# Performance work log

Hardware: AMD Instinct MI355X
Metric: run time of the kernel (lower is better)

Reference implementation:

```python
import jax, jax.numpy as jnp
import numpy as np

H_GRID = 512
W_GRID = 512
N_NODES = H_GRID * W_GRID


def gcn_conv(x, W, b, src, dst, n):
    # PyG GCNConv: linear transform, add self-loops, symmetric normalization,
    # scatter-add aggregation, bias.
    h = x @ W  # [N, F_out]
    # degree including self-loop (edge weights are all 1)
    deg = jax.ops.segment_sum(jnp.ones(src.shape[0], x.dtype), dst, num_segments=n) + 1.0
    dinv = jax.lax.rsqrt(deg)  # deg^-0.5
    norm = dinv[src] * dinv[dst]  # [E]
    msg = h[src] * norm[:, None]  # [E, F_out] gathered messages
    agg = jax.ops.segment_sum(msg, dst, num_segments=n)
    # self-loop contribution: norm_ii = deg_i^-0.5 * deg_i^-0.5 = 1/deg_i
    agg = agg + h * (dinv * dinv)[:, None]
    return agg + b


def setup_inputs() -> dict:
    key = jax.random.key(0)
    k_x, k_w1, k_w2, k_wfc = jax.random.split(key, 4)

    # 4-neighbor grid edges (both directions), matching build_grid_edges
    ii, jj = np.meshgrid(np.arange(H_GRID), np.arange(W_GRID), indexing='ij')
    idx = (ii * W_GRID + jj).astype(np.int32)
    src_h, dst_h = idx[:, :-1].ravel(), idx[:, 1:].ravel()
    src_v, dst_v = idx[:-1, :].ravel(), idx[1:, :].ravel()
    src = np.concatenate([src_h, dst_h, src_v, dst_v])
    dst = np.concatenate([dst_h, src_h, dst_v, src_v])
    edge_index = jnp.asarray(np.stack([src, dst]), dtype=jnp.int32)  # [2, E]

    x = jax.random.normal(k_x, (N_NODES, 2), dtype=jnp.float32)
    s1 = 1.0 / np.sqrt(2.0)
    s2 = 1.0 / np.sqrt(64.0)
    W1 = jax.random.uniform(k_w1, (2, 64), jnp.float32, -s1, s1)
    b1 = jnp.zeros((64,), jnp.float32)
    W2 = jax.random.uniform(k_w2, (64, 64), jnp.float32, -s2, s2)
    b2 = jnp.zeros((64,), jnp.float32)
    Wfc = jax.random.uniform(k_wfc, (64, 1), jnp.float32, -s2, s2)
    bfc = jnp.zeros((1,), jnp.float32)
    return {"x": x, "edge_index": edge_index, "W1": W1, "b1": b1,
            "W2": W2, "b2": b2, "Wfc": Wfc, "bfc": bfc}


def reference(x, edge_index, W1, b1, W2, b2, Wfc, bfc):
    src, dst = edge_index[0], edge_index[1]
    n = x.shape[0]
    h = jax.nn.relu(gcn_conv(x, W1, b1, src, dst, n))
    h = jax.nn.relu(gcn_conv(h, W2, b2, src, dst, n))
    out = jax.nn.sigmoid(h @ Wfc + bfc)  # [N, 1]
    return out.squeeze(-1)  # [N]
```

## Files before the change

kernel.cpp:

```cpp
#include <hip/hip_runtime.h>
#include <hip/hip_fp16.h>
#include <math.h>

#define HG 512
#define WG 512
#define F 64
#define TS 16
#define HS 18
#define HN (HS * HS)

typedef _Float16 f16x8 __attribute__((ext_vector_type(8)));
typedef __fp16 fp16x2 __attribute__((ext_vector_type(2)));
typedef __attribute__((ext_vector_type(4))) float f32x4;

__device__ __forceinline__ float dinv_of(int r, int c) {
    int nb = (r > 0) + (r < HG - 1) + (c > 0) + (c < WG - 1);
    return nb == 4 ? 0.4472135954999579f : (nb == 3 ? 0.5f : 0.5773502691896258f);
}

__device__ __forceinline__ int swz(int row, int ch) {
    int key = (row ^ (row >> 3)) & 7;
    return row * 128 + ((ch ^ key) << 4);
}

__device__ __forceinline__ __half2 bch2(unsigned u) { return __builtin_bit_cast(__half2, u); }

__global__ __launch_bounds__(1024, 8) void fused(const float* __restrict__ x,
                                                 const float* __restrict__ W1,
                                                 const float* __restrict__ b1,
                                                 const float* __restrict__ W2,
                                                 const float* __restrict__ b2,
                                                 const float* __restrict__ Wfc,
                                                 const float* __restrict__ bfc,
                                                 float* __restrict__ out) {
    __shared__ unsigned short Hs[HN * 64];
    __shared__ unsigned short WT[64 * 64];
    __shared__ float2 a1s[HN];

    char* hb = (char*)Hs;
    char* wb = (char*)WT;
    int tid = threadIdx.x;
    int tr = blockIdx.x >> 5, tc = blockIdx.x & 31;
    int r0 = tr * TS, c0 = tc * TS;

    for (int i = tid; i < 64 * 64; i += 1024) {
        int k = i >> 6, n = i & 63;
        *(_Float16*)(wb + swz(n, k >> 3) + (k & 7) * 2) = (_Float16)W2[i];
    }

    const float2* xv = (const float2*)x;
    if (tid < HN) {
        int node = tid;
        int lr = (node * 57) >> 10;
        int lc = node - lr * 18;
        int rT = r0 - 1 + lr, cT = c0 - 1 + lc;
        float s0 = 0.f, s1 = 0.f;
        if (rT >= 0 && rT < HG && cT >= 0 && cT < WG) {
            int n = (rT << 9) + cT;
            float di = dinv_of(rT, cT);
            float2 v = xv[n];
            s0 = di * di * v.x; s1 = di * di * v.y;
            if (cT > 0)      { float w = di * dinv_of(rT, cT - 1); float2 t = xv[n - 1];  s0 += w * t.x; s1 += w * t.y; }
            if (cT < WG - 1) { float w = di * dinv_of(rT, cT + 1); float2 t = xv[n + 1];  s0 += w * t.x; s1 += w * t.y; }
            if (rT > 0)      { float w = di * dinv_of(rT - 1, cT); float2 t = xv[n - WG]; s0 += w * t.x; s1 += w * t.y; }
            if (rT < HG - 1) { float w = di * dinv_of(rT + 1, cT); float2 t = xv[n + WG]; s0 += w * t.x; s1 += w * t.y; }
        }
        a1s[node] = make_float2(s0, s1);
    }

    int fq = tid & 15;
    float4 w0 = ((const float4*)W1)[fq];
    float4 w1 = ((const float4*)(W1 + 64))[fq];
    float4 bb = ((const float4*)b1)[fq];
    __syncthreads();
    for (int node = (tid >> 4); node < HN; node += 64) {
        float2 a = a1s[node];
        float h0 = fmaxf(fmaf(a.x, w0.x, fmaf(a.y, w1.x, bb.x)), 0.f);
        float h1v = fmaxf(fmaf(a.x, w0.y, fmaf(a.y, w1.y, bb.y)), 0.f);
        float h2 = fmaxf(fmaf(a.x, w0.z, fmaf(a.y, w1.z, bb.z)), 0.f);
        float h3 = fmaxf(fmaf(a.x, w0.w, fmaf(a.y, w1.w, bb.w)), 0.f);
        fp16x2 p0 = __builtin_amdgcn_cvt_pkrtz(h0, h1v);
        fp16x2 p1 = __builtin_amdgcn_cvt_pkrtz(h2, h3);
        uint2 pk;
        pk.x = __builtin_bit_cast(unsigned, p0);
        pk.y = __builtin_bit_cast(unsigned, p1);
        *(uint2*)(hb + swz(node, fq >> 1) + (fq & 1) * 8) = pk;
    }
    __syncthreads();

    int wv = tid >> 6, lane = tid & 63;
    int q = lane >> 4, col = lane & 15;

    int lr = wv + 1, lc = col + 1;
    int rT = r0 + wv, cT = c0 + col;
    float di = dinv_of(rT, cT);
    __half2 wc2 = __half2half2(__float2half(di * di));
    __half2 wl2 = __half2half2(__float2half((cT > 0)      ? di * dinv_of(rT, cT - 1) : 0.f));
    __half2 wr2 = __half2half2(__float2half((cT < WG - 1) ? di * dinv_of(rT, cT + 1) : 0.f));
    __half2 wu2 = __half2half2(__float2half((rT > 0)      ? di * dinv_of(rT - 1, cT) : 0.f));
    __half2 wd2 = __half2half2(__float2half((rT < HG - 1) ? di * dinv_of(rT + 1, cT) : 0.f));
    int hrow = lr * HS + lc;

    f16x8 af[2];
    #pragma unroll
    for (int ck = 0; ck < 2; ck++) {
        int c = ck * 4 + q;
        uint4 vc = *(const uint4*)(hb + swz(hrow, c));
        uint4 vl = *(const uint4*)(hb + swz(hrow - 1, c));
        uint4 vr = *(const uint4*)(hb + swz(hrow + 1, c));
        uint4 vu = *(const uint4*)(hb + swz(hrow - HS, c));
        uint4 vd = *(const uint4*)(hb + swz(hrow + HS, c));
        const unsigned* pc = (const unsigned*)&vc;
        const unsigned* pl = (const unsigned*)&vl;
        const unsigned* pr = (const unsigned*)&vr;
        const unsigned* pu = (const unsigned*)&vu;
        const unsigned* pd = (const unsigned*)&vd;
        unsigned res[4];
        #pragma unroll
        for (int u = 0; u < 4; u++) {
            __half2 a = __hmul2(bch2(pc[u]), wc2);
            a = __hfma2(bch2(pl[u]), wl2, a);
            a = __hfma2(bch2(pr[u]), wr2, a);
            a = __hfma2(bch2(pu[u]), wu2, a);
            a = __hfma2(bch2(pd[u]), wd2, a);
            res[u] = __builtin_bit_cast(unsigned, a);
        }
        uint4 r4 = {res[0], res[1], res[2], res[3]};
        af[ck] = __builtin_bit_cast(f16x8, r4);
    }

    float p[4] = {0.f, 0.f, 0.f, 0.f};
    #pragma unroll
    for (int nt = 0; nt < 4; nt++) {
        f16x8 bf0 = *(const f16x8*)(wb + swz(nt * 16 + col, q));
        f16x8 bf1 = *(const f16x8*)(wb + swz(nt * 16 + col, 4 + q));
        f32x4 z = {0.f, 0.f, 0.f, 0.f};
        z = __builtin_amdgcn_mfma_f32_16x16x32_f16(af[0], bf0, z, 0, 0, 0);
        z = __builtin_amdgcn_mfma_f32_16x16x32_f16(af[1], bf1, z, 0, 0, 0);
        float b2v = b2[nt * 16 + col];
        float wfv = Wfc[nt * 16 + col];
        #pragma unroll
        for (int rg = 0; rg < 4; rg++)
            p[rg] += fmaxf(z[rg] + b2v, 0.f) * wfv;
    }
    #pragma unroll
    for (int rg = 0; rg < 4; rg++) {
        #pragma unroll
        for (int s = 1; s < 16; s <<= 1)
            p[rg] += __shfl_xor(p[rg], s, 64);
    }
    if (col == 0) {
        float bfc0 = bfc[0];
        #pragma unroll
        for (int rg = 0; rg < 4; rg++) {
            int nT = (r0 + wv) * WG + c0 + q * 4 + rg;
            float zz = p[rg] + bfc0;
            out[nT] = 1.f / (1.f + expf(-zz));
        }
    }
}

extern "C" void kernel_launch(void* const* d_in, const int* in_sizes, int n_in,
                              void* d_out, int out_size, void* d_ws, size_t ws_size,
                              hipStream_t stream) {
    const float* x   = (const float*)d_in[0];
    const float* W1  = (const float*)d_in[2];
    const float* b1  = (const float*)d_in[3];
    const float* W2  = (const float*)d_in[4];
    const float* b2  = (const float*)d_in[5];
    const float* Wfc = (const float*)d_in[6];
    const float* bfc = (const float*)d_in[7];
    float* out = (float*)d_out;

    fused<<<(HG / TS) * (WG / TS), 1024, 0, stream>>>(x, W1, b1, W2, b2, Wfc, bfc, out);
}
```

Baseline: 86.66 us.

## Fuse layer-1 aggregation and transform, dropping the intermediate LDS buffer and barrier

Each thread now computes the 2-channel layer-1 aggregate for a node and directly applies W1, bias and ReLU for 8 output features, writing fp16 to the swizzled H tile. This removes the a1s shared buffer and one __syncthreads. Each node's aggregate is recomputed by 8 threads, adding redundant global loads and arithmetic. The W2 load is also vectorised as one float4 per thread and issued early to overlap with the stencil work.

```diff
diff --git a/kernel.cpp b/kernel.cpp
--- a/kernel.cpp
+++ b/kernel.cpp
@@ -24,6 +24,10 @@
 }
 
 __device__ __forceinline__ __half2 bch2(unsigned u) { return __builtin_bit_cast(__half2, u); }
+__device__ __forceinline__ unsigned pkrtz(float a, float b) {
+    fp16x2 p = __builtin_amdgcn_cvt_pkrtz(a, b);
+    return __builtin_bit_cast(unsigned, p);
+}
 
 __global__ __launch_bounds__(1024, 8) void fused(const float* __restrict__ x,
                                                  const float* __restrict__ W1,
@@ -35,7 +39,6 @@
                                                  float* __restrict__ out) {
     __shared__ unsigned short Hs[HN * 64];
     __shared__ unsigned short WT[64 * 64];
-    __shared__ float2 a1s[HN];
 
     char* hb = (char*)Hs;
     char* wb = (char*)WT;
@@ -43,55 +46,65 @@
     int tr = blockIdx.x >> 5, tc = blockIdx.x & 31;
     int r0 = tr * TS, c0 = tc * TS;
 
-    for (int i = tid; i < 64 * 64; i += 1024) {
-        int k = i >> 6, n = i & 63;
-        *(_Float16*)(wb + swz(n, k >> 3) + (k & 7) * 2) = (_Float16)W2[i];
+    float4 w2v = ((const float4*)W2)[tid];
+
+    int fh = tid & 7;
+    float4 wA0 = ((const float4*)W1)[2 * fh];
+    float4 wA1 = ((const float4*)W1)[2 * fh + 1];
+    float4 wB0 = ((const float4*)(W1 + 64))[2 * fh];
+    float4 wB1 = ((const float4*)(W1 + 64))[2 * fh + 1];
+    float4 bb0 = ((const float4*)b1)[2 * fh];
+    float4 bb1 = ((const float4*)b1)[2 * fh + 1];
+
+    const float2* xv = (const float2*)x;
+    #pragma unroll
+    for (int j = 0; j < 3; j++) {
+        int item = tid + j * 1024;
+        if (item < HN * 8) {
+            int node = item >> 3;
+            int lr = (node * 57) >> 10;
+            int lc = node - lr * 18;
+            int rT = r0 - 1 + lr, cT = c0 - 1 + lc;
+            float s0 = 0.f, s1 = 0.f;
+            if (rT >= 0 && rT < HG && cT >= 0 && cT < WG) {
+                int n = (rT << 9) + cT;
+                float di = dinv_of(rT, cT);
+                float2 v = xv[n];
+                s0 = di * di * v.x; s1 = di * di * v.y;
+                if (cT > 0)      { float w = di * dinv_of(rT, cT - 1); float2 t = xv[n - 1];  s0 += w * t.x; s1 += w * t.y; }
+                if (cT < WG - 1) { float w = di * dinv_of(rT, cT + 1); float2 t = xv[n + 1];  s0 += w * t.x; s1 += w * t.y; }
+                if (rT > 0)      { float w = di * dinv_of(rT - 1, cT); float2 t = xv[n - WG]; s0 += w * t.x; s1 += w * t.y; }
+                if (rT < HG - 1) { float w = di * dinv_of(rT + 1, cT); float2 t = xv[n + WG]; s0 += w * t.x; s1 += w * t.y; }
+            }
+            float h0 = fmaxf(fmaf(s0, wA0.x, fmaf(s1, wB0.x, bb0.x)), 0.f);
+            float h1v = fmaxf(fmaf(s0, wA0.y, fmaf(s1, wB0.y, bb0.y)), 0.f);
+            float h2 = fmaxf(fmaf(s0, wA0.z, fmaf(s1, wB0.z, bb0.z)), 0.f);
+            float h3 = fmaxf(fmaf(s0, wA0.w, fmaf(s1, wB0.w, bb0.w)), 0.f);
+            float h4 = fmaxf(fmaf(s0, wA1.x, fmaf(s1, wB1.x, bb1.x)), 0.f);
+            float h5 = fmaxf(fmaf(s0, wA1.y, fmaf(s1, wB1.y, bb1.y)), 0.f);
+            float h6 = fmaxf(fmaf(s0, wA1.z, fmaf(s1, wB1.z, bb1.z)), 0.f);
+            float h7 = fmaxf(fmaf(s0, wA1.w, fmaf(s1, wB1.w, bb1.w)), 0.f);
+            uint4 pk4;
+            pk4.x = pkrtz(h0, h1v);
+            pk4.y = pkrtz(h2, h3);
+            pk4.z = pkrtz(h4, h5);
+            pk4.w = pkrtz(h6, h7);
+            *(uint4*)(hb + swz(node, fh)) = pk4;
+        }
     }
 
-    const float2* xv = (const float2*)x;
-    if (tid < HN) {
-        int node = tid;
-        int lr = (node * 57) >> 10;
-        int lc = node - lr * 18;
-        int rT = r0 - 1 + lr, cT = c0 - 1 + lc;
-        float s0 = 0.f, s1 = 0.f;
-        if (rT >= 0 && rT < HG && cT >= 0 && cT < WG) {
-            int n = (rT << 9) + cT;
-            float di = dinv_of(rT, cT);
-            float2 v = xv[n];
-            s0 = di * di * v.x; s1 = di * di * v.y;
-            if (cT > 0)      { float w = di * dinv_of(rT, cT - 1); float2 t = xv[n - 1];  s0 += w * t.x; s1 += w * t.y; }
-            if (cT < WG - 1) { float w = di * dinv_of(rT, cT + 1); float2 t = xv[n + 1];  s0 += w * t.x; s1 += w * t.y; }
-            if (rT > 0)      { float w = di * dinv_of(rT - 1, cT); float2 t = xv[n - WG]; s0 += w * t.x; s1 += w * t.y; }
-            if (rT < HG - 1) { float w = di * dinv_of(rT + 1, cT); float2 t = xv[n + WG]; s0 += w * t.x; s1 += w * t.y; }
-        }
-        a1s[node] = make_float2(s0, s1);
-    }
-
-    int fq = tid & 15;
-    float4 w0 = ((const float4*)W1)[fq];
-    float4 w1 = ((const float4*)(W1 + 64))[fq];
-    float4 bb = ((const float4*)b1)[fq];
-    __syncthreads();
-    for (int node = (tid >> 4); node < HN; node += 64) {
-        float2 a = a1s[node];
-        float h0 = fmaxf(fmaf(a.x, w0.x, fmaf(a.y, w1.x, bb.x)), 0.f);
-        float h1v = fmaxf(fmaf(a.x, w0.y, fmaf(a.y, w1.y, bb.y)), 0.f);
-        float h2 = fmaxf(fmaf(a.x, w0.z, fmaf(a.y, w1.z, bb.z)), 0.f);
-        float h3 = fmaxf(fmaf(a.x, w0.w, fmaf(a.y, w1.w, bb.w)), 0.f);
-        fp16x2 p0 = __builtin_amdgcn_cvt_pkrtz(h0, h1v);
-        fp16x2 p1 = __builtin_amdgcn_cvt_pkrtz(h2, h3);
-        uint2 pk;
-        pk.x = __builtin_bit_cast(unsigned, p0);
-        pk.y = __builtin_bit_cast(unsigned, p1);
-        *(uint2*)(hb + swz(node, fq >> 1) + (fq & 1) * 8) = pk;
+    {
+        int k = tid >> 4, n0 = (tid & 15) * 4;
+        *(_Float16*)(wb + swz(n0 + 0, k >> 3) + (k & 7) * 2) = (_Float16)w2v.x;
+        *(_Float16*)(wb + swz(n0 + 1, k >> 3) + (k & 7) * 2) = (_Float16)w2v.y;
+        *(_Float16*)(wb + swz(n0 + 2, k >> 3) + (k & 7) * 2) = (_Float16)w2v.z;
+        *(_Float16*)(wb + swz(n0 + 3, k >> 3) + (k & 7) * 2) = (_Float16)w2v.w;
     }
     __syncthreads();
 
     int wv = tid >> 6, lane = tid & 63;
     int q = lane >> 4, col = lane & 15;
 
-    int lr = wv + 1, lc = col + 1;
     int rT = r0 + wv, cT = c0 + col;
     float di = dinv_of(rT, cT);
     __half2 wc2 = __half2half2(__float2half(di * di));
@@ -99,7 +112,7 @@
     __half2 wr2 = __half2half2(__float2half((cT < WG - 1) ? di * dinv_of(rT, cT + 1) : 0.f));
     __half2 wu2 = __half2half2(__float2half((rT > 0)      ? di * dinv_of(rT - 1, cT) : 0.f));
     __half2 wd2 = __half2half2(__float2half((rT < HG - 1) ? di * dinv_of(rT + 1, cT) : 0.f));
-    int hrow = lr * HS + lc;
+    int hrow = (wv + 1) * HS + (col + 1);
 
     f16x8 af[2];
     #pragma unroll
```

After: 91.52 us. 5.6% more time.
